# Optimization experiments

Hardware: AMD Instinct MI355X
Metric: run time of the kernel (lower is better)

The kernel has to match this reference:

```python
import jax, jax.numpy as jnp
import numpy as np

PERM = (0, 3, 2, 1, 4)  # self-inverse permutation used by the module


def setup_inputs() -> dict:
    key = jax.random.key(0)
    k1, k2, k3 = jax.random.split(key, 3)
    shape = (2, 32, 80, 80, 80)  # [B, C, H, W, D]
    return {
        "x_": jax.random.normal(k1, shape, dtype=jnp.float32),
        "x_t": jax.random.normal(k2, shape, dtype=jnp.float32),
        "g_x": jax.random.normal(k3, shape, dtype=jnp.float32),
    }


def reference(x_, x_t, g_x):
    B = x_.shape[0]
    W = x_.shape[3]  # coronal size (attention sequence length)
    # permute to [B, W, H, C, D], flatten feature dims -> [B, W, K]
    q = jnp.transpose(x_, PERM).reshape(B, W, -1)
    k = jnp.transpose(x_t, PERM).reshape(B, W, -1)
    gv5 = jnp.transpose(g_x, PERM)
    ori = gv5.shape  # (B, W, H, C, D)
    v = gv5.reshape(B, W, -1)
    # unscaled attention over coronal slices: [B, W, W]
    att = jax.nn.softmax(jnp.einsum("bwk,bvk->bwv", q, k), axis=-1)
    out = jnp.einsum("bwv,bvk->bwk", att, v)
    out = out.reshape(ori)
    # permute back to [B, C, H, W, D]
    return jnp.transpose(out, PERM)
```

## Files before the change

### kernel.cpp

```cpp
#include <hip/hip_runtime.h>
#include <math.h>


#define BB 2
#define CC 32
#define HH 80
#define WW 80
#define DD 80
#define CH (CC*HH)
#define SLICE (WW*DD)
#define PAD 84

__global__ __launch_bounds__(256, 2)
void qk_kernel(const float* __restrict__ x, const float* __restrict__ xt,
               float* __restrict__ S) {
  __shared__ __align__(16) float Xs[WW][PAD];
  __shared__ __align__(16) float Ts[WW][PAD];
  const int blk = blockIdx.x;
  const int b = blk >> 9;
  const int chunk = blk & 511;
  const int tid = threadIdx.x;
  const int ty = tid >> 4, tx = tid & 15;

  float acc[5][5] = {};
  const long base = (long)(b * CH + chunk * 5) * SLICE;

  for (int s = 0; s < 5; ++s) {
    const float* px = x  + base + (long)s * SLICE;
    const float* pt = xt + base + (long)s * SLICE;
    __syncthreads();
    for (int i = tid; i < SLICE; i += 256) {
      int w = i / DD, d = i - w * DD;
      Xs[w][d] = px[i];
      Ts[w][d] = pt[i];
    }
    __syncthreads();
    for (int d = 0; d < DD; d += 4) {
      float a[5][4], t[5][4];
      #pragma unroll
      for (int i = 0; i < 5; ++i) {
        float4 v4 = *(const float4*)&Xs[ty + 16 * i][d];
        a[i][0] = v4.x; a[i][1] = v4.y; a[i][2] = v4.z; a[i][3] = v4.w;
      }
      #pragma unroll
      for (int j = 0; j < 5; ++j) {
        float4 v4 = *(const float4*)&Ts[tx + 16 * j][d];
        t[j][0] = v4.x; t[j][1] = v4.y; t[j][2] = v4.z; t[j][3] = v4.w;
      }
      #pragma unroll
      for (int r = 0; r < 4; ++r)
        #pragma unroll
        for (int i = 0; i < 5; ++i)
          #pragma unroll
          for (int j = 0; j < 5; ++j)
            acc[i][j] = fmaf(a[i][r], t[j][r], acc[i][j]);
    }
  }

  float* Sb = S + b * WW * WW;
  #pragma unroll
  for (int i = 0; i < 5; ++i)
    #pragma unroll
    for (int j = 0; j < 5; ++j)
      atomicAdd(&Sb[(ty + 16 * i) * WW + tx + 16 * j], acc[i][j]);
}

__global__ void softmax_kernel(float* __restrict__ S) {
  const int r = blockIdx.x;
  const int lane = threadIdx.x;
  float* row = S + r * WW;
  float v0 = (lane < WW) ? row[lane] : -INFINITY;
  float v1 = (lane + 64 < WW) ? row[lane + 64] : -INFINITY;
  float m = fmaxf(v0, v1);
  #pragma unroll
  for (int off = 32; off; off >>= 1) m = fmaxf(m, __shfl_xor(m, off));
  float e0 = (lane < WW) ? expf(v0 - m) : 0.f;
  float e1 = (lane + 64 < WW) ? expf(v1 - m) : 0.f;
  float ssum = e0 + e1;
  #pragma unroll
  for (int off = 32; off; off >>= 1) ssum += __shfl_xor(ssum, off);
  float inv = 1.f / ssum;
  if (lane < WW) row[lane] = e0 * inv;
  if (lane + 64 < WW) row[lane + 64] = e1 * inv;
}

__global__ __launch_bounds__(256, 2)
void pv_kernel(const float* __restrict__ g, const float* __restrict__ att,
               float* __restrict__ out) {
  __shared__ __align__(16) float As[WW][PAD];
  __shared__ __align__(16) float Gs[WW][PAD];
  const int blk = blockIdx.x;
  const int tid = threadIdx.x;
  const int ty = tid >> 4, tx = tid & 15;
  const int s0 = blk * 2;
  const int b = s0 / CH;

  const float* ab = att + b * WW * WW;
  for (int i = tid; i < WW * WW; i += 256) {
    int w = i / WW;
    As[w][i - w * WW] = ab[i];
  }

  for (int s = 0; s < 2; ++s) {
    const long base = (long)(s0 + s) * SLICE;
    const float* pg = g + base;
    __syncthreads();
    for (int i = tid; i < SLICE; i += 256) {
      int w = i / DD;
      Gs[w][i - w * DD] = pg[i];
    }
    __syncthreads();

    float acc[5][5] = {};
    for (int v = 0; v < WW; v += 4) {
      float a[5][4];
      #pragma unroll
      for (int i = 0; i < 5; ++i) {
        float4 v4 = *(const float4*)&As[ty + 16 * i][v];
        a[i][0] = v4.x; a[i][1] = v4.y; a[i][2] = v4.z; a[i][3] = v4.w;
      }
      #pragma unroll
      for (int r = 0; r < 4; ++r) {
        float gv[5];
        #pragma unroll
        for (int j = 0; j < 5; ++j) gv[j] = Gs[v + r][tx + 16 * j];
        #pragma unroll
        for (int i = 0; i < 5; ++i)
          #pragma unroll
          for (int j = 0; j < 5; ++j)
            acc[i][j] = fmaf(a[i][r], gv[j], acc[i][j]);
      }
    }

    float* po = out + base;
    #pragma unroll
    for (int i = 0; i < 5; ++i)
      #pragma unroll
      for (int j = 0; j < 5; ++j)
        po[(ty + 16 * i) * DD + tx + 16 * j] = acc[i][j];
  }
}

extern "C" void kernel_launch(void* const* d_in, const int* in_sizes, int n_in,
                              void* d_out, int out_size, void* d_ws, size_t ws_size,
                              hipStream_t stream) {
  const float* x_  = (const float*)d_in[0];
  const float* x_t = (const float*)d_in[1];
  const float* g_x = (const float*)d_in[2];
  float* out = (float*)d_out;
  float* S = (float*)d_ws;

  hipMemsetAsync(S, 0, BB * WW * WW * sizeof(float), stream);
  qk_kernel<<<dim3(1024), dim3(256), 0, stream>>>(x_, x_t, S);
  softmax_kernel<<<dim3(BB * WW), dim3(64), 0, stream>>>(S);
  pv_kernel<<<dim3(2560), dim3(256), 0, stream>>>(g_x, S, out);
}
```

Before: 481.2 us.

## Rewrite QK and PV kernels with per-wave 10x10 register tiles and prefetch

Both GEMM kernels are rebuilt so that each wavefront owns whole slices and computes a 10x10 register tile per thread. The K dimension is streamed in 16-wide chunks through per-wave LDS buffers, and the next chunk is prefetched into registers while the current one is computed. QK partial sums are first reduced across waves in LDS, so fewer global atomics are issued, and the grid shrinks to 512 blocks. The larger tiles raise register pressure and lower parallelism, and the split of 2 or 3 slices per wave may leave waves unevenly loaded.

```diff
diff --git a/kernel.cpp b/kernel.cpp
--- a/kernel.cpp
+++ b/kernel.cpp
@@ -2,73 +2,138 @@
 #include <math.h>
 
 
-#define BB 2
-#define CC 32
-#define HH 80
 #define WW 80
 #define DD 80
-#define CH (CC*HH)
-#define SLICE (WW*DD)
-#define PAD 84
+#define SLICE 6400
+#define SPB 2560
+#define CPAD 20
 
 __global__ __launch_bounds__(256, 2)
-void qk_kernel(const float* __restrict__ x, const float* __restrict__ xt,
-               float* __restrict__ S) {
-  __shared__ __align__(16) float Xs[WW][PAD];
-  __shared__ __align__(16) float Ts[WW][PAD];
-  const int blk = blockIdx.x;
-  const int b = blk >> 9;
-  const int chunk = blk & 511;
-  const int tid = threadIdx.x;
-  const int ty = tid >> 4, tx = tid & 15;
-
-  float acc[5][5] = {};
-  const long base = (long)(b * CH + chunk * 5) * SLICE;
-
-  for (int s = 0; s < 5; ++s) {
-    const float* px = x  + base + (long)s * SLICE;
-    const float* pt = xt + base + (long)s * SLICE;
-    __syncthreads();
-    for (int i = tid; i < SLICE; i += 256) {
-      int w = i / DD, d = i - w * DD;
-      Xs[w][d] = px[i];
-      Ts[w][d] = pt[i];
+void qk2_kernel(const float* __restrict__ x, const float* __restrict__ xt,
+                float* __restrict__ S) {
+  __shared__ __align__(16) float lds[4][2][WW][CPAD];
+  const int tid  = threadIdx.x;
+  const int wv   = tid >> 6;
+  const int lane = tid & 63;
+  const int r    = lane >> 3;
+  const int c    = lane & 7;
+  const int bi   = blockIdx.x;
+
+  const int ns = 2 + ((bi + wv) & 1);
+  const int s0 = bi * 10 + 2 * wv + ((wv + (bi & 1)) >> 1);
+  const int batch = (bi * 10) / SPB;
+
+  float* Xc = &lds[wv][0][0][0];
+  float* Tc = &lds[wv][1][0][0];
+
+  const int row0 = lane >> 2;
+  const int c4   = lane & 3;
+
+  float acc[10][10] = {};
+
+  float4 px[5], pt[5];
+  {
+    const float* pbx = x  + (long)s0 * SLICE + c4 * 4;
+    const float* pbt = xt + (long)s0 * SLICE + c4 * 4;
+    #pragma unroll
+    for (int t = 0; t < 5; ++t) {
+      px[t] = *(const float4*)(pbx + (row0 + 16 * t) * DD);
+      pt[t] = *(const float4*)(pbt + (row0 + 16 * t) * DD);
     }
-    __syncthreads();
-    for (int d = 0; d < DD; d += 4) {
-      float a[5][4], t[5][4];
-      #pragma unroll
-      for (int i = 0; i < 5; ++i) {
-        float4 v4 = *(const float4*)&Xs[ty + 16 * i][d];
-        a[i][0] = v4.x; a[i][1] = v4.y; a[i][2] = v4.z; a[i][3] = v4.w;
-      }
-      #pragma unroll
-      for (int j = 0; j < 5; ++j) {
-        float4 v4 = *(const float4*)&Ts[tx + 16 * j][d];
-        t[j][0] = v4.x; t[j][1] = v4.y; t[j][2] = v4.z; t[j][3] = v4.w;
-      }
-      #pragma unroll
-      for (int r = 0; r < 4; ++r)
-        #pragma unroll
-        for (int i = 0; i < 5; ++i)
-          #pragma unroll
-          for (int j = 0; j < 5; ++j)
-            acc[i][j] = fmaf(a[i][r], t[j][r], acc[i][j]);
+  }
+
+  for (int s = 0; s < ns; ++s) {
+    for (int ch = 0; ch < 5; ++ch) {
+      #pragma unroll
+      for (int t = 0; t < 5; ++t) {
+        *(float4*)(Xc + (row0 + 16 * t) * CPAD + c4 * 4) = px[t];
+        *(float4*)(Tc + (row0 + 16 * t) * CPAD + c4 * 4) = pt[t];
+      }
+      {
+        int s2 = s, ch2 = ch + 1;
+        if (ch2 == 5) { ch2 = 0; s2 = s + 1; }
+        if (s2 < ns) {
+          const float* pbx = x  + (long)(s0 + s2) * SLICE + ch2 * 16 + c4 * 4;
+          const float* pbt = xt + (long)(s0 + s2) * SLICE + ch2 * 16 + c4 * 4;
+          #pragma unroll
+          for (int t = 0; t < 5; ++t) {
+            px[t] = *(const float4*)(pbx + (row0 + 16 * t) * DD);
+            pt[t] = *(const float4*)(pbt + (row0 + 16 * t) * DD);
+          }
+        }
+      }
+      #pragma unroll 2
+      for (int kk = 0; kk < 16; kk += 2) {
+        float2 a[10], bb[10];
+        #pragma unroll
+        for (int i = 0; i < 10; ++i)
+          a[i] = *(const float2*)(Xc + (r * 10 + i) * CPAD + kk);
+        #pragma unroll
+        for (int j = 0; j < 10; ++j)
+          bb[j] = *(const float2*)(Tc + (c * 10 + j) * CPAD + kk);
+        #pragma unroll
+        for (int i = 0; i < 10; ++i)
+          #pragma unroll
+          for (int j = 0; j < 10; ++j) {
+            acc[i][j] = fmaf(a[i].x, bb[j].x, acc[i][j]);
+            acc[i][j] = fmaf(a[i].y, bb[j].y, acc[i][j]);
+          }
+      }
     }
   }
 
-  float* Sb = S + b * WW * WW;
-  #pragma unroll
-  for (int i = 0; i < 5; ++i)
-    #pragma unroll
-    for (int j = 0; j < 5; ++j)
-      atomicAdd(&Sb[(ty + 16 * i) * WW + tx + 16 * j], acc[i][j]);
+  float* flat = &lds[0][0][0][0];
+  __syncthreads();
+  if (wv & 1) {
+    float* reg = flat + (wv >> 1) * SLICE;
+    #pragma unroll
+    for (int i = 0; i < 10; ++i)
+      #pragma unroll
+      for (int p = 0; p < 5; ++p) {
+        float2 v = { acc[i][2 * p], acc[i][2 * p + 1] };
+        *(float2*)(reg + (r * 10 + i) * WW + c * 10 + 2 * p) = v;
+      }
+  }
+  __syncthreads();
+  if (!(wv & 1)) {
+    const float* reg = flat + (wv >> 1) * SLICE;
+    #pragma unroll
+    for (int i = 0; i < 10; ++i)
+      #pragma unroll
+      for (int p = 0; p < 5; ++p) {
+        float2 v = *(const float2*)(reg + (r * 10 + i) * WW + c * 10 + 2 * p);
+        acc[i][2 * p]     += v.x;
+        acc[i][2 * p + 1] += v.y;
+      }
+  }
+  __syncthreads();
+  if (wv == 2) {
+    #pragma unroll
+    for (int i = 0; i < 10; ++i)
+      #pragma unroll
+      for (int p = 0; p < 5; ++p) {
+        float2 v = { acc[i][2 * p], acc[i][2 * p + 1] };
+        *(float2*)(flat + (r * 10 + i) * WW + c * 10 + 2 * p) = v;
+      }
+  }
+  __syncthreads();
+  if (wv == 0) {
+    float* Sb = S + batch * SLICE;
+    #pragma unroll
+    for (int i = 0; i < 10; ++i)
+      #pragma unroll
+      for (int p = 0; p < 5; ++p) {
+        float2 v = *(const float2*)(flat + (r * 10 + i) * WW + c * 10 + 2 * p);
+        atomicAdd(&Sb[(r * 10 + i) * WW + c * 10 + 2 * p],     acc[i][2 * p]     + v.x);
+        atomicAdd(&Sb[(r * 10 + i) * WW + c * 10 + 2 * p + 1], acc[i][2 * p + 1] + v.y);
+      }
+  }
 }
 
 __global__ void softmax_kernel(float* __restrict__ S) {
-  const int r = blockIdx.x;
+  const int rr = blockIdx.x;
   const int lane = threadIdx.x;
-  float* row = S + r * WW;
+  float* row = S + rr * WW;
   float v0 = (lane < WW) ? row[lane] : -INFINITY;
   float v1 = (lane + 64 < WW) ? row[lane + 64] : -INFINITY;
   float m = fmaxf(v0, v1);
@@ -85,59 +150,88 @@
 }
 
 __global__ __launch_bounds__(256, 2)
-void pv_kernel(const float* __restrict__ g, const float* __restrict__ att,
-               float* __restrict__ out) {
-  __shared__ __align__(16) float As[WW][PAD];
-  __shared__ __align__(16) float Gs[WW][PAD];
-  const int blk = blockIdx.x;
-  const int tid = threadIdx.x;
-  const int ty = tid >> 4, tx = tid & 15;
-  const int s0 = blk * 2;
-  const int b = s0 / CH;
-
-  const float* ab = att + b * WW * WW;
-  for (int i = tid; i < WW * WW; i += 256) {
-    int w = i / WW;
-    As[w][i - w * WW] = ab[i];
-  }
-
-  for (int s = 0; s < 2; ++s) {
-    const long base = (long)(s0 + s) * SLICE;
-    const float* pg = g + base;
-    __syncthreads();
-    for (int i = tid; i < SLICE; i += 256) {
-      int w = i / DD;
-      Gs[w][i - w * DD] = pg[i];
+void pv2_kernel(const float* __restrict__ g, const float* __restrict__ att,
+                float* __restrict__ out) {
+  __shared__ __align__(16) float As[WW][84];
+  __shared__ __align__(16) float Gc[4][16][84];
+  const int tid  = threadIdx.x;
+  const int wv   = tid >> 6;
+  const int lane = tid & 63;
+  const int r    = lane >> 3;
+  const int c    = lane & 7;
+  const int bi   = blockIdx.x;
+
+  const int ns = 2 + ((bi + wv) & 1);
+  const int s0 = bi * 10 + 2 * wv + ((wv + (bi & 1)) >> 1);
+  const int batch = (bi * 10) / SPB;
+
+  const float* ab = att + batch * SLICE;
+  for (int f = tid; f < 1600; f += 256) {
+    int row = f / 20, c4f = f - row * 20;
+    *(float4*)(&As[row][c4f * 4]) = *(const float4*)(ab + row * WW + c4f * 4);
+  }
+  __syncthreads();
+
+  float* Gw = &Gc[wv][0][0];
+  const int vrow = lane >> 2;
+  const int c4   = lane & 3;
+
+  float4 pg[5];
+  {
+    const float* pb = g + (long)s0 * SLICE + vrow * DD + c4 * 4;
+    #pragma unroll
+    for (int t = 0; t < 5; ++t)
+      pg[t] = *(const float4*)(pb + 16 * t);
+  }
+
+  for (int s = 0; s < ns; ++s) {
+    float acc[10][10] = {};
+    for (int ch = 0; ch < 5; ++ch) {
+      #pragma unroll
+      for (int t = 0; t < 5; ++t)
+        *(float4*)(Gw + vrow * 84 + (c4 + 4 * t) * 4) = pg[t];
+      {
+        int s2 = s, ch2 = ch + 1;
+        if (ch2 == 5) { ch2 = 0; s2 = s + 1; }
+        if (s2 < ns) {
+          const float* pb = g + (long)(s0 + s2) * SLICE + (ch2 * 16 + vrow) * DD + c4 * 4;
+          #pragma unroll
+          for (int t = 0; t < 5; ++t)
+            pg[t] = *(const float4*)(pb + 16 * t);
+        }
+      }
+      const int v0 = ch * 16;
+      #pragma unroll 2
+      for (int kk = 0; kk < 16; kk += 2) {
+        float2 a[10];
+        #pragma unroll
+        for (int i = 0; i < 10; ++i)
+          a[i] = *(const float2*)(&As[r * 10 + i][v0 + kk]);
+        float2 gA[5], gB[5];
+        #pragma unroll
+        for (int p = 0; p < 5; ++p) {
+          gA[p] = *(const float2*)(Gw + kk * 84 + c * 10 + 2 * p);
+          gB[p] = *(const float2*)(Gw + (kk + 1) * 84 + c * 10 + 2 * p);
+        }
+        #pragma unroll
+        for (int i = 0; i < 10; ++i)
+          #pragma unroll
+          for (int p = 0; p < 5; ++p) {
+            acc[i][2 * p]     = fmaf(a[i].x, gA[p].x, acc[i][2 * p]);
+            acc[i][2 * p + 1] = fmaf(a[i].x, gA[p].y, acc[i][2 * p + 1]);
+            acc[i][2 * p]     = fmaf(a[i].y, gB[p].x, acc[i][2 * p]);
+            acc[i][2 * p + 1] = fmaf(a[i].y, gB[p].y, acc[i][2 * p + 1]);
+          }
+      }
     }
-    __syncthreads();
-
-    float acc[5][5] = {};
-    for (int v = 0; v < WW; v += 4) {
-      float a[5][4];
-      #pragma unroll
-      for (int i = 0; i < 5; ++i) {
-        float4 v4 = *(const float4*)&As[ty + 16 * i][v];
-        a[i][0] = v4.x; a[i][1] = v4.y; a[i][2] = v4.z; a[i][3] = v4.w;
-      }
-      #pragma unroll
-      for (int r = 0; r < 4; ++r) {
-        float gv[5];
-        #pragma unroll
-        for (int j = 0; j < 5; ++j) gv[j] = Gs[v + r][tx + 16 * j];
-        #pragma unroll
-        for (int i = 0; i < 5; ++i)
-          #pragma unroll
-          for (int j = 0; j < 5; ++j)
-            acc[i][j] = fmaf(a[i][r], gv[j], acc[i][j]);
-      }
-    }
-
-    float* po = out + base;
-    #pragma unroll
-    for (int i = 0; i < 5; ++i)
-      #pragma unroll
-      for (int j = 0; j < 5; ++j)
-        po[(ty + 16 * i) * DD + tx + 16 * j] = acc[i][j];
+    float* po = out + (long)(s0 + s) * SLICE;
+    #pragma unroll
+    for (int i = 0; i < 10; ++i)
+      #pragma unroll
+      for (int p = 0; p < 5; ++p) {
+        float2 v = { acc[i][2 * p], acc[i][2 * p + 1] };
+        *(float2*)(po + (r * 10 + i) * DD + c * 10 + 2 * p) = v;
+      }
   }
 }
 
@@ -150,8 +244,8 @@
   float* out = (float*)d_out;
   float* S = (float*)d_ws;
 
-  hipMemsetAsync(S, 0, BB * WW * WW * sizeof(float), stream);
-  qk_kernel<<<dim3(1024), dim3(256), 0, stream>>>(x_, x_t, S);
-  softmax_kernel<<<dim3(BB * WW), dim3(64), 0, stream>>>(S);
-  pv_kernel<<<dim3(2560), dim3(256), 0, stream>>>(g_x, S, out);
-}
+  hipMemsetAsync(S, 0, 2 * SLICE * sizeof(float), stream);
+  qk2_kernel<<<dim3(512), dim3(256), 0, stream>>>(x_, x_t, S);
+  softmax_kernel<<<dim3(160), dim3(64), 0, stream>>>(S);
+  pv2_kernel<<<dim3(512), dim3(256), 0, stream>>>(g_x, S, out);
+}
```

New measurement: 711.6 us. 47.9% more time.
